# Optimization experiments

Measured on AMD Instinct MI355X. Metric: run time of the kernel, lower is better.

Reference implementation:

```python
import jax, jax.numpy as jnp
import numpy as np

SEQ_LEN, BATCH, HID, ATT = 2048, 64, 512, 512


def setup_inputs() -> dict:
    key = jax.random.key(0)
    k1, k2, k3, k4, k5, k6 = jax.random.split(key, 6)
    return {
        "dec_out": jax.random.normal(k1, (BATCH, HID), dtype=jnp.float32),
        "enc_outs": jax.random.normal(k2, (SEQ_LEN, BATCH, HID), dtype=jnp.float32),
        "W_s": jax.random.normal(k3, (ATT, HID), dtype=jnp.float32) * (1.0 / np.sqrt(HID)),
        "W_t": jax.random.normal(k4, (ATT, HID), dtype=jnp.float32) * (1.0 / np.sqrt(HID)),
        "b_t": jax.random.normal(k5, (ATT,), dtype=jnp.float32) * 0.01,
        "v_a": jax.random.uniform(k6, (ATT,), dtype=jnp.float32, minval=-0.05, maxval=0.05),
    }


def reference(dec_out, enc_outs, W_s, W_t, b_t, v_a):
    # enc_att: (seq_len, batch, att) = W_s @ enc_outs
    enc_att = jnp.einsum('sbh,ah->sba', enc_outs, W_s)
    # dec_att: (batch, att) = W_t @ dec_out + b_t
    dec_att = dec_out @ W_t.T + b_t
    # score(b, s) = v_a . tanh(enc_att[s,b] + dec_att[b])
    scores = jnp.einsum('sba,a->bs', jnp.tanh(enc_att + dec_att[None, :, :]), v_a)
    return scores  # (batch, seq_len)
```

## Files before the change

### kernel.cpp

```cpp
#include <hip/hip_runtime.h>

typedef __attribute__((ext_vector_type(8))) short short8;
typedef __attribute__((ext_vector_type(4))) float f32x4;

#define SEQ 2048
#define BATCH 64
#define HID 512
#define ATT 512
#define SPB 8

__device__ __forceinline__ unsigned short f2bf(float f) {
  unsigned u = __float_as_uint(f);
  u += 0x7fffu + ((u >> 16) & 1u);
  return (unsigned short)(u >> 16);
}

__global__ void bahdanau_pre(const float* __restrict__ dec_out,
                             const float* __restrict__ W_t,
                             const float* __restrict__ b_t,
                             const float* __restrict__ W_s,
                             unsigned short* __restrict__ wsb,
                             float* __restrict__ decT) {
  if (blockIdx.x < 64) {
    const int b = blockIdx.x;
    __shared__ float drow[HID];
    for (int i = threadIdx.x; i < HID; i += 256) drow[i] = dec_out[b * HID + i];
    __syncthreads();
    for (int a = threadIdx.x; a < ATT; a += 256) {
      const float4* wr = (const float4*)(W_t + (size_t)a * HID);
      float s0 = 0.f, s1 = 0.f, s2 = 0.f, s3 = 0.f;
#pragma unroll 4
      for (int j = 0; j < HID / 4; ++j) {
        float4 w = wr[j];
        s0 = fmaf(w.x, drow[4 * j + 0], s0);
        s1 = fmaf(w.y, drow[4 * j + 1], s1);
        s2 = fmaf(w.z, drow[4 * j + 2], s2);
        s3 = fmaf(w.w, drow[4 * j + 3], s3);
      }
      decT[a * BATCH + b] = (s0 + s1) + (s2 + s3) + b_t[a];
    }
  } else {
    const int cb = blockIdx.x - 64;
    const float4* src = (const float4*)W_s;
#pragma unroll
    for (int i = 0; i < 4; ++i) {
      int idx = cb * 1024 + i * 256 + threadIdx.x;
      float4 v = src[idx];
      ushort4 o;
      o.x = f2bf(v.x); o.y = f2bf(v.y); o.z = f2bf(v.z); o.w = f2bf(v.w);
      ((ushort4*)wsb)[idx] = o;
    }
  }
}

__global__ __launch_bounds__(512, 2)
void bahdanau_main(const float* __restrict__ enc,
                   const unsigned short* __restrict__ wsb,
                   const float* __restrict__ decT,
                   const float* __restrict__ v_a,
                   float* __restrict__ out) {
  __shared__ __align__(16) unsigned short Albuf[2][16 * 4 * 65 * 8];
  __shared__ float partial[2][512];

  const int tid  = threadIdx.x;
  const int wave = tid >> 6;
  const int lane = tid & 63;
  const int c = lane & 15;
  const int q = lane >> 4;
  const int n0 = wave * 64;
  const int s0 = blockIdx.x * SPB;

  const int srow = tid >> 3;
  const int skc  = (tid & 7) * 4;
  const int ldst = (((skc >> 3) & 3) * 65 + srow) * 8 + (skc & 7);
  const float* gbase = enc + ((size_t)s0 * 64 + srow) * HID + skc;

  const unsigned short* bsrc = wsb + (size_t)(n0 + c) * HID + q * 8;

  float va[4];
#pragma unroll
  for (int nt = 0; nt < 4; ++nt) va[nt] = v_a[n0 + nt * 16 + c];

#pragma unroll 1
  for (int g = 0; g < 4; ++g) {
    float4 v[4];
#pragma unroll
    for (int u = 0; u < 4; ++u) v[u] = *(const float4*)(gbase + (g * 4 + u) * 32);
#pragma unroll
    for (int u = 0; u < 4; ++u) {
      ushort4 o;
      o.x = f2bf(v[u].x); o.y = f2bf(v[u].y); o.z = f2bf(v[u].z); o.w = f2bf(v[u].w);
      *(ushort4*)&Albuf[0][(g * 4 + u) * 2080 + ldst] = o;
    }
  }
  __syncthreads();

#pragma unroll 1
  for (int si = 0; si < SPB; ++si) {
    unsigned short* Acur = Albuf[si & 1];
    unsigned short* Anxt = Albuf[(si & 1) ^ 1];
    const bool more = (si + 1 < SPB);
    const float* gnext = gbase + (size_t)(si + 1) * (64 * HID);

    f32x4 acc[4][4];
#pragma unroll
    for (int nt = 0; nt < 4; ++nt)
#pragma unroll
      for (int mt = 0; mt < 4; ++mt)
        acc[mt][nt] = *(const f32x4*)(decT + (size_t)(n0 + nt * 16 + c) * 64 + mt * 16 + q * 4);

    short8 bp[2][4];
#pragma unroll
    for (int d = 0; d < 2; ++d)
#pragma unroll
      for (int nt = 0; nt < 4; ++nt)
        bp[d][nt] = *(const short8*)(bsrc + nt * 16 * HID + d * 32);

    float4 stg[4];
    if (more) {
#pragma unroll
      for (int u = 0; u < 4; ++u) stg[u] = *(const float4*)(gnext + u * 32);
    }

#pragma unroll 1
    for (int g = 0; g < 4; ++g) {
#pragma unroll
      for (int u = 0; u < 4; ++u) {
        const int kk = g * 4 + u;

        const unsigned short* ab = &Acur[kk * 2080 + (q * 65 + c) * 8];
        short8 a4[4];
#pragma unroll
        for (int mt = 0; mt < 4; ++mt)
          a4[mt] = *(const short8*)(ab + mt * 128);

#pragma unroll
        for (int mt = 0; mt < 4; ++mt)
#pragma unroll
          for (int nt = 0; nt < 4; ++nt)
            acc[mt][nt] = __builtin_amdgcn_mfma_f32_16x16x32_bf16(a4[mt], bp[u & 1][nt], acc[mt][nt], 0, 0, 0);

#pragma unroll
        for (int nt = 0; nt < 4; ++nt)
          bp[u & 1][nt] = *(const short8*)(bsrc + nt * 16 * HID + (kk + 2) * 32);

        if (more) {
          ushort4 o;
          o.x = f2bf(stg[u].x); o.y = f2bf(stg[u].y);
          o.z = f2bf(stg[u].z); o.w = f2bf(stg[u].w);
          *(ushort4*)&Anxt[kk * 2080 + ldst] = o;
          if (kk < 12) stg[u] = *(const float4*)(gnext + (kk + 4) * 32);
        }
      }
    }

    float rowsum[4][4];
#pragma unroll
    for (int mt = 0; mt < 4; ++mt) {
#pragma unroll
      for (int r = 0; r < 4; ++r) {
        float sum = 0.f;
#pragma unroll
        for (int nt = 0; nt < 4; ++nt) {
          float x = acc[mt][nt][r];
          float e = __builtin_amdgcn_exp2f(x * 2.8853900817779268f);
          float t = 1.f - 2.f * __builtin_amdgcn_rcpf(e + 1.f);
          sum = fmaf(va[nt], t, sum);
        }
        rowsum[mt][r] = sum;
      }
    }

#pragma unroll
    for (int off = 1; off < 16; off <<= 1) {
#pragma unroll
      for (int mt = 0; mt < 4; ++mt)
#pragma unroll
        for (int r = 0; r < 4; ++r)
          rowsum[mt][r] += __shfl_xor(rowsum[mt][r], off, 64);
    }

    if (c == 0) {
#pragma unroll
      for (int mt = 0; mt < 4; ++mt)
#pragma unroll
        for (int r = 0; r < 4; ++r)
          partial[si & 1][wave * 64 + mt * 16 + q * 4 + r] = rowsum[mt][r];
    }

    __syncthreads();

    if (tid < 64) {
      float sum = 0.f;
#pragma unroll
      for (int w = 0; w < 8; ++w) sum += partial[si & 1][w * 64 + tid];
      out[(size_t)tid * SEQ + s0 + si] = sum;
    }
  }
}

extern "C" void kernel_launch(void* const* d_in, const int* in_sizes, int n_in,
                              void* d_out, int out_size, void* d_ws, size_t ws_size,
                              hipStream_t stream) {
  const float* dec_out = (const float*)d_in[0];
  const float* enc     = (const float*)d_in[1];
  const float* W_s     = (const float*)d_in[2];
  const float* W_t     = (const float*)d_in[3];
  const float* b_t     = (const float*)d_in[4];
  const float* v_a     = (const float*)d_in[5];
  float* out = (float*)d_out;

  unsigned short* wsb = (unsigned short*)d_ws;
  float* decT = (float*)((char*)d_ws + (size_t)ATT * HID * 2);

  bahdanau_pre<<<128, 256, 0, stream>>>(dec_out, W_t, b_t, W_s, wsb, decT);
  bahdanau_main<<<SEQ / SPB, 512, 0, stream>>>(enc, wsb, decT, v_a, out);
}
```

Before: 523.6 us.

## Use 1024-thread blocks with 32 attention columns per wave and bulk prefetch

After: 550.3 us. +5.1%, slower.

```diff
diff --git a/kernel.cpp b/kernel.cpp
--- a/kernel.cpp
+++ b/kernel.cpp
@@ -53,105 +53,94 @@
   }
 }
 
-__global__ __launch_bounds__(512, 2)
+__global__ __launch_bounds__(1024, 4)
 void bahdanau_main(const float* __restrict__ enc,
                    const unsigned short* __restrict__ wsb,
                    const float* __restrict__ decT,
                    const float* __restrict__ v_a,
                    float* __restrict__ out) {
-  __shared__ __align__(16) unsigned short Albuf[2][16 * 4 * 65 * 8];
-  __shared__ float partial[2][512];
+  __shared__ __align__(16) unsigned short Albuf[2][16 * 2080];
+  __shared__ float partial[2][16 * 64];
 
   const int tid  = threadIdx.x;
   const int wave = tid >> 6;
   const int lane = tid & 63;
   const int c = lane & 15;
   const int q = lane >> 4;
-  const int n0 = wave * 64;
+  const int n0 = wave * 32;
   const int s0 = blockIdx.x * SPB;
 
-  const int srow = tid >> 3;
-  const int skc  = (tid & 7) * 4;
-  const int ldst = (((skc >> 3) & 3) * 65 + srow) * 8 + (skc & 7);
-  const float* gbase = enc + ((size_t)s0 * 64 + srow) * HID + skc;
+  const int row = tid >> 4;
+  const int t15 = tid & 15;
+  const float* gbase = enc + ((size_t)s0 * 64 + row) * HID + t15 * 4;
+  const int ldbase = (t15 >> 3) * 2080 + (((t15 >> 1) & 3) * 65 + row) * 8 + (t15 & 1) * 4;
 
   const unsigned short* bsrc = wsb + (size_t)(n0 + c) * HID + q * 8;
 
-  float va[4];
-#pragma unroll
-  for (int nt = 0; nt < 4; ++nt) va[nt] = v_a[n0 + nt * 16 + c];
-
-#pragma unroll 1
-  for (int g = 0; g < 4; ++g) {
-    float4 v[4];
-#pragma unroll
-    for (int u = 0; u < 4; ++u) v[u] = *(const float4*)(gbase + (g * 4 + u) * 32);
-#pragma unroll
-    for (int u = 0; u < 4; ++u) {
+  float va[2] = { v_a[n0 + c], v_a[n0 + 16 + c] };
+
+  {
+    float4 v[8];
+#pragma unroll
+    for (int j = 0; j < 8; ++j) v[j] = *(const float4*)(gbase + j * 64);
+#pragma unroll
+    for (int j = 0; j < 8; ++j) {
       ushort4 o;
-      o.x = f2bf(v[u].x); o.y = f2bf(v[u].y); o.z = f2bf(v[u].z); o.w = f2bf(v[u].w);
-      *(ushort4*)&Albuf[0][(g * 4 + u) * 2080 + ldst] = o;
+      o.x = f2bf(v[j].x); o.y = f2bf(v[j].y); o.z = f2bf(v[j].z); o.w = f2bf(v[j].w);
+      *(ushort4*)&Albuf[0][j * 4160 + ldbase] = o;
     }
   }
   __syncthreads();
 
 #pragma unroll 1
   for (int si = 0; si < SPB; ++si) {
-    unsigned short* Acur = Albuf[si & 1];
-    unsigned short* Anxt = Albuf[(si & 1) ^ 1];
-    const bool more = (si + 1 < SPB);
-    const float* gnext = gbase + (size_t)(si + 1) * (64 * HID);
-
-    f32x4 acc[4][4];
-#pragma unroll
-    for (int nt = 0; nt < 4; ++nt)
+    const int cur = si & 1;
+
+    f32x4 acc[4][2];
+#pragma unroll
+    for (int nt = 0; nt < 2; ++nt)
 #pragma unroll
       for (int mt = 0; mt < 4; ++mt)
         acc[mt][nt] = *(const f32x4*)(decT + (size_t)(n0 + nt * 16 + c) * 64 + mt * 16 + q * 4);
 
-    short8 bp[2][4];
+    short8 bp[2][2];
 #pragma unroll
     for (int d = 0; d < 2; ++d)
 #pragma unroll
-      for (int nt = 0; nt < 4; ++nt)
+      for (int nt = 0; nt < 2; ++nt)
         bp[d][nt] = *(const short8*)(bsrc + nt * 16 * HID + d * 32);
 
-    float4 stg[4];
-    if (more) {
-#pragma unroll
-      for (int u = 0; u < 4; ++u) stg[u] = *(const float4*)(gnext + u * 32);
-    }
-
-#pragma unroll 1
-    for (int g = 0; g < 4; ++g) {
-#pragma unroll
-      for (int u = 0; u < 4; ++u) {
-        const int kk = g * 4 + u;
-
-        const unsigned short* ab = &Acur[kk * 2080 + (q * 65 + c) * 8];
-        short8 a4[4];
-#pragma unroll
-        for (int mt = 0; mt < 4; ++mt)
-          a4[mt] = *(const short8*)(ab + mt * 128);
-
-#pragma unroll
-        for (int mt = 0; mt < 4; ++mt)
-#pragma unroll
-          for (int nt = 0; nt < 4; ++nt)
-            acc[mt][nt] = __builtin_amdgcn_mfma_f32_16x16x32_bf16(a4[mt], bp[u & 1][nt], acc[mt][nt], 0, 0, 0);
-
-#pragma unroll
-        for (int nt = 0; nt < 4; ++nt)
-          bp[u & 1][nt] = *(const short8*)(bsrc + nt * 16 * HID + (kk + 2) * 32);
-
-        if (more) {
-          ushort4 o;
-          o.x = f2bf(stg[u].x); o.y = f2bf(stg[u].y);
-          o.z = f2bf(stg[u].z); o.w = f2bf(stg[u].w);
-          *(ushort4*)&Anxt[kk * 2080 + ldst] = o;
-          if (kk < 12) stg[u] = *(const float4*)(gnext + (kk + 4) * 32);
-        }
-      }
+    const int sil = (si + 1 < SPB) ? si + 1 : si;
+    const float* gnext = gbase + (size_t)sil * (64 * HID);
+    float4 stg[8];
+#pragma unroll
+    for (int j = 0; j < 8; ++j) stg[j] = *(const float4*)(gnext + j * 64);
+
+#pragma unroll
+    for (int kk = 0; kk < 16; ++kk) {
+      const unsigned short* ab = &Albuf[cur][kk * 2080 + (q * 65 + c) * 8];
+      short8 a4[4];
+#pragma unroll
+      for (int mt = 0; mt < 4; ++mt)
+        a4[mt] = *(const short8*)(ab + mt * 128);
+
+#pragma unroll
+      for (int mt = 0; mt < 4; ++mt)
+#pragma unroll
+        for (int nt = 0; nt < 2; ++nt)
+          acc[mt][nt] = __builtin_amdgcn_mfma_f32_16x16x32_bf16(a4[mt], bp[kk & 1][nt], acc[mt][nt], 0, 0, 0);
+
+#pragma unroll
+      for (int nt = 0; nt < 2; ++nt)
+        bp[kk & 1][nt] = *(const short8*)(bsrc + nt * 16 * HID + (kk + 2) * 32);
+    }
+
+#pragma unroll
+    for (int j = 0; j < 8; ++j) {
+      ushort4 o;
+      o.x = f2bf(stg[j].x); o.y = f2bf(stg[j].y);
+      o.z = f2bf(stg[j].z); o.w = f2bf(stg[j].w);
+      *(ushort4*)&Albuf[cur ^ 1][j * 4160 + ldbase] = o;
     }
 
     float rowsum[4][4];
@@ -161,7 +150,7 @@
       for (int r = 0; r < 4; ++r) {
         float sum = 0.f;
 #pragma unroll
-        for (int nt = 0; nt < 4; ++nt) {
+        for (int nt = 0; nt < 2; ++nt) {
           float x = acc[mt][nt][r];
           float e = __builtin_amdgcn_exp2f(x * 2.8853900817779268f);
           float t = 1.f - 2.f * __builtin_amdgcn_rcpf(e + 1.f);
@@ -193,7 +182,7 @@
     if (tid < 64) {
       float sum = 0.f;
 #pragma unroll
-      for (int w = 0; w < 8; ++w) sum += partial[si & 1][w * 64 + tid];
+      for (int w = 0; w < 16; ++w) sum += partial[si & 1][w * 64 + tid];
       out[(size_t)tid * SEQ + s0 + si] = sum;
     }
   }
@@ -214,5 +203,5 @@
   float* decT = (float*)((char*)d_ws + (size_t)ATT * HID * 2);
 
   bahdanau_pre<<<128, 256, 0, stream>>>(dec_out, W_t, b_t, W_s, wsb, decT);
-  bahdanau_main<<<SEQ / SPB, 512, 0, stream>>>(enc, wsb, decT, v_a, out);
-}
+  bahdanau_main<<<SEQ / SPB, 1024, 0, stream>>>(enc, wsb, decT, v_a, out);
+}
```
